# Kernel optimization log

Measured on AMD Instinct MI355X. Metric: run time of the kernel, lower is better.

The kernel has to match this reference:

```python
import jax, jax.numpy as jnp
import numpy as np

B, H, W, C = 2, 64, 64, 512
GROUPS = 32
EPS = 1e-5


def group_norm(x, gamma, beta):
    b, h, w, c = x.shape
    xg = x.reshape(b, h, w, GROUPS, c // GROUPS)
    mu = xg.mean(axis=(1, 2, 4), keepdims=True)
    var = xg.var(axis=(1, 2, 4), keepdims=True)
    xn = ((xg - mu) * jax.lax.rsqrt(var + EPS)).reshape(b, h, w, c)
    return xn * gamma + beta


def setup_inputs() -> dict:
    key = jax.random.key(0)
    ks = jax.random.split(key, 12)
    wscale = 0.02
    inputs = jax.random.normal(ks[0], (B, H, W, C), jnp.float32)
    gamma = jnp.ones((C,), jnp.float32)
    beta = jnp.zeros((C,), jnp.float32)
    Wq = jax.random.normal(ks[1], (C, C), jnp.float32) * wscale
    bq = jnp.zeros((C,), jnp.float32)
    Wk = jax.random.normal(ks[2], (C, C), jnp.float32) * wscale
    bk = jnp.zeros((C,), jnp.float32)
    Wv = jax.random.normal(ks[3], (C, C), jnp.float32) * wscale
    bv = jnp.zeros((C,), jnp.float32)
    Wp = jax.random.normal(ks[4], (C, C), jnp.float32) * wscale
    bp = jnp.zeros((C,), jnp.float32)
    return {"inputs": inputs, "gamma": gamma, "beta": beta,
            "Wq": Wq, "bq": bq, "Wk": Wk, "bk": bk,
            "Wv": Wv, "bv": bv, "Wp": Wp, "bp": bp}


def reference(inputs, gamma, beta, Wq, bq, Wk, bk, Wv, bv, Wp, bp):
    b, h, w, c = inputs.shape
    x = group_norm(inputs, gamma, beta)
    # QKV projections on [b, h, w, c], flatten spatial to sequence hw
    q = (x @ Wq + bq).reshape(b, h * w, c)
    k = (x @ Wk + bk).reshape(b, h * w, c)
    v = (x @ Wv + bv).reshape(b, h * w, c)
    scale = 1.0 / jnp.sqrt(jnp.asarray(c, q.dtype))
    # y[b,i,j] = <q_i, k_j> / sqrt(c); softmax over keys j (last axis, keras default)
    attn = jax.nn.softmax(jnp.einsum('bqc,bkc->bqk', q, k) * scale, axis=-1)
    # out_i = sum_j attn[i,j] * v_j  (matches v @ y^T in the original)
    o = jnp.einsum('bqk,bkc->bqc', attn, v).reshape(b, h, w, c)
    return (o @ Wp + bp) + inputs
```

## Files before the change

### kernel.cpp

```cpp
#include <hip/hip_runtime.h>
#include <hip/hip_bf16.h>
#include <cstddef>


typedef __bf16 bf16;
typedef __attribute__((ext_vector_type(8))) __bf16 bf16x8;
typedef __attribute__((ext_vector_type(4))) __bf16 bf16x4;
typedef __attribute__((ext_vector_type(4))) float f32x4;

#define SEQ   4096
#define CCH   512
#define NBAT  2
#define NOMASK 0x7FFFFFFF
#define SMEM_BYTES 32768

__device__ __forceinline__ void prep_unit(
    char* smem, int bid, const float* __restrict__ x,
    const float* __restrict__ Wq, const float* __restrict__ Wk,
    const float* __restrict__ Wv, const float* __restrict__ Wp,
    const float* __restrict__ bq, const float* __restrict__ bk,
    const float* __restrict__ bv,
    float* __restrict__ statsP, bf16* __restrict__ WqkvT,
    bf16* __restrict__ WpT, float* __restrict__ biasQKV) {
    const int tid = threadIdx.x;
    if (bid < 512) {
        float* red = (float*)smem;
        int bg = bid >> 3, c = bid & 7;
        int b = bg >> 5, g = bg & 31;
        const float* base = x + (size_t)b * SEQ * CCH + g * 16;
        float s = 0.f, ss = 0.f;
        for (int i = tid; i < 2048; i += 256) {
            int sp = c * 512 + (i >> 2), q = i & 3;
            float4 v = *(const float4*)(base + (size_t)sp * CCH + q * 4);
            s  += v.x + v.y + v.z + v.w;
            ss += v.x * v.x + v.y * v.y + v.z * v.z + v.w * v.w;
        }
        #pragma unroll
        for (int o = 32; o > 0; o >>= 1) { s += __shfl_down(s, o); ss += __shfl_down(ss, o); }
        int wave = tid >> 6, lane = tid & 63;
        if (lane == 0) { red[wave] = s; red[4 + wave] = ss; }
        __syncthreads();
        if (tid == 0) {
            statsP[bg * 16 + c]     = red[0] + red[1] + red[2] + red[3];
            statsP[bg * 16 + 8 + c] = red[4] + red[5] + red[6] + red[7];
        }
        __syncthreads();
    } else if (bid < 1536) {
        float (*tile)[33] = (float(*)[33])smem;
        int w = bid - 512;
        int z = w >> 8, rest = w & 255;
        int k0 = (rest >> 4) * 32, n0 = (rest & 15) * 32;
        const float* W = (z == 0) ? Wq : (z == 1) ? Wk : (z == 2) ? Wv : Wp;
        int tx = tid & 31, ty = tid >> 5;
        #pragma unroll
        for (int i = ty; i < 32; i += 8)
            tile[i][tx] = W[(size_t)(k0 + i) * CCH + n0 + tx];
        __syncthreads();
        bf16* dst = (z < 3) ? (WqkvT + (size_t)z * CCH * CCH) : WpT;
        #pragma unroll
        for (int i = ty; i < 32; i += 8)
            dst[(size_t)(n0 + i) * CCH + k0 + tx] = (bf16)tile[tx][i];
        __syncthreads();
    } else {
        for (int i = tid; i < 1536; i += 256) {
            float v = (i < 512) ? bq[i] : (i < 1024) ? bk[i - 512] : bv[i - 1024];
            biasQKV[i] = v;
        }
    }
}

__device__ __forceinline__ void gn_table(char* smem, const float* __restrict__ statsP) {
    float* tbl = (float*)smem;
    const int tid = threadIdx.x;
    if (tid < 64) {
        float S = 0.f, SS = 0.f;
        #pragma unroll
        for (int c = 0; c < 8; ++c) { S += statsP[tid * 16 + c]; SS += statsP[tid * 16 + 8 + c]; }
        float mu = S * (1.f / 65536.f);
        float rs = rsqrtf(SS * (1.f / 65536.f) - mu * mu + 1e-5f);
        tbl[tid * 2] = mu; tbl[tid * 2 + 1] = rs;
    }
    __syncthreads();
}

__device__ __forceinline__ void gn_unit(
    char* smem, int w, const float* __restrict__ x,
    const float* __restrict__ gamma, const float* __restrict__ beta,
    bf16* __restrict__ xn) {
    const float* tbl = (const float*)smem;
    size_t idx = (size_t)w * 256 + threadIdx.x;
    int c4 = (int)(idx & 127);
    int b = (int)(idx >> 19);
    int bg = b * 32 + (c4 >> 2);
    float mu = tbl[bg * 2], rs = tbl[bg * 2 + 1];
    float4 v  = ((const float4*)x)[idx];
    float4 gm = ((const float4*)gamma)[c4];
    float4 bt = ((const float4*)beta)[c4];
    bf16x4 o;
    o[0] = (bf16)((v.x - mu) * rs * gm.x + bt.x);
    o[1] = (bf16)((v.y - mu) * rs * gm.y + bt.y);
    o[2] = (bf16)((v.z - mu) * rs * gm.z + bt.z);
    o[3] = (bf16)((v.w - mu) * rs * gm.w + bt.w);
    ((bf16x4*)xn)[idx] = o;
}

__device__ __forceinline__ void vtrans_unit(char* smem,
                                            const bf16* __restrict__ qkv,
                                            bf16* __restrict__ vT,
                                            int b, int s0, int c0) {
    bf16 (*tile)[65] = (bf16(*)[65])smem;
    const int tx = threadIdx.x & 63;
    const int w = threadIdx.x >> 6;
    #pragma unroll
    for (int i = 0; i < 16; ++i) {
        int row = w + i * 4;
        tile[row][tx] = qkv[((size_t)b * SEQ + s0 + row) * 1536 + 1024 + c0 + tx];
    }
    __syncthreads();
    #pragma unroll
    for (int i = 0; i < 16; ++i) {
        int row = w + i * 4;
        vT[((size_t)b * CCH + c0 + row) * SEQ + s0 + tx] = tile[tx][row];
    }
    __syncthreads();
}

template <int EPI, int BN>
__device__ __forceinline__ void gemm2_body(
    char* smem, int bxi, int byi, int bzi,
    const bf16* __restrict__ A, long long aBatch, int lda,
    const bf16* __restrict__ Bt, long long bBatch, int ldb,
    void* __restrict__ Cout, long long cBatch, int ldc,
    int K, int bkmask, float scale,
    const float* __restrict__ bias, const float* __restrict__ resid,
    float* __restrict__ lsum, long long lsumBatch) {
    constexpr int JN = BN / 32;
    bf16* As = (bf16*)smem;
    bf16* Bs = (bf16*)(smem + 16384);
    const int tid = threadIdx.x;
    const int lane = tid & 63;
    const int wave = tid >> 6;

    int zb = bzi, kc = 0;
    if constexpr (EPI == 2) { kc = zb & 1; zb >>= 1; }
    const long long m0 = (long long)bxi * 128;
    const long long n0 = (long long)byi * BN;
    const bf16* Ab = A + (long long)zb * aBatch + (EPI == 2 ? (long long)kc * 2048 : 0);
    const bf16* Bb = Bt + (long long)zb * bBatch + (EPI == 2 ? (long long)kc * 2048 : 0);

    const int wm = (wave & 1) * 64;
    const int wn = (wave >> 1) * (BN / 2);
    const int fm = lane & 15;
    const int q4 = lane >> 4;

    f32x4 acc[4][JN];
    #pragma unroll
    for (int i = 0; i < 4; ++i)
        #pragma unroll
        for (int j = 0; j < JN; ++j)
            acc[i][j] = (f32x4){0.f, 0.f, 0.f, 0.f};

    const int srow = tid >> 3;
    const int schunk = (tid & 7) ^ (srow & 7);

    for (int k0 = 0; k0 < K; k0 += 64) {
        const int kA = k0 + schunk * 8;
        const int kB = (k0 & bkmask) + schunk * 8;
        #pragma unroll
        for (int cb = 0; cb < 4; ++cb) {
            const bf16* g = Ab + (m0 + cb * 32 + srow) * (long long)lda + kA;
            __builtin_amdgcn_global_load_lds((const __attribute__((address_space(1))) void*)g,
                                             (__attribute__((address_space(3))) void*)&As[cb * 2048 + tid * 8], 16, 0, 0);
        }
        #pragma unroll
        for (int cb = 0; cb < BN / 32; ++cb) {
            const bf16* g = Bb + (n0 + cb * 32 + srow) * (long long)ldb + kB;
            __builtin_amdgcn_global_load_lds((const __attribute__((address_space(1))) void*)g,
                                             (__attribute__((address_space(3))) void*)&Bs[cb * 2048 + tid * 8], 16, 0, 0);
        }
        __syncthreads();
        #pragma unroll
        for (int kcc = 0; kcc < 2; ++kcc) {
            bf16x8 fa[4], fb[JN];
            #pragma unroll
            for (int i = 0; i < 4; ++i) {
                const int row = wm + i * 16 + fm;
                const int sw = ((kcc * 4 + q4) ^ (fm & 7)) * 8;
                fa[i] = *(const bf16x8*)&As[row * 64 + sw];
            }
            #pragma unroll
            for (int j = 0; j < JN; ++j) {
                const int row = wn + j * 16 + fm;
                const int sw = ((kcc * 4 + q4) ^ (fm & 7)) * 8;
                fb[j] = *(const bf16x8*)&Bs[row * 64 + sw];
            }
            #pragma unroll
            for (int i = 0; i < 4; ++i)
                #pragma unroll
                for (int j = 0; j < JN; ++j)
                    acc[i][j] = __builtin_amdgcn_mfma_f32_16x16x32_bf16(fa[i], fb[j], acc[i][j], 0, 0, 0);
        }
        __syncthreads();
    }

    float* lrow = (float*)(smem + 1024);
    if constexpr (EPI == 2) {
        float* lscr = (float*)smem;
        const float* lsb = lsum + (long long)zb * lsumBatch + m0;
        const int row = tid & 127, h = tid >> 7;
        float s = 0.f;
        #pragma unroll
        for (int p = 0; p < 32; ++p)
            s += lsb[(long long)(h * 32 + p) * SEQ + row];
        lscr[tid] = s;
        __syncthreads();
        if (tid < 128) lrow[tid] = 1.f / (lscr[tid] + lscr[tid + 128]);
        __syncthreads();
    }

    const int col = lane & 15;
    const int rowb = (lane >> 4) * 4;

    if constexpr (EPI == 1) {
        bf16* Pb = (bf16*)Cout + (long long)zb * cBatch;
        float* lsw = lsum + (long long)zb * lsumBatch
                   + ((long long)byi * 2 + (wave >> 1)) * SEQ;
        #pragma unroll
        for (int i = 0; i < 4; ++i) {
            float rs[4] = {0.f, 0.f, 0.f, 0.f};
            long long mg = m0 + wm + i * 16 + rowb;
            #pragma unroll
            for (int j = 0; j < JN; ++j) {
                long long ng = n0 + wn + j * 16 + col;
                #pragma unroll
                for (int r = 0; r < 4; ++r) {
                    float e = __expf(acc[i][j][r] * scale);
                    rs[r] += e;
                    Pb[(mg + r) * (long long)ldc + ng] = (bf16)e;
                }
            }
            #pragma unroll
            for (int r = 0; r < 4; ++r) {
                rs[r] += __shfl_xor(rs[r], 1);
                rs[r] += __shfl_xor(rs[r], 2);
                rs[r] += __shfl_xor(rs[r], 4);
                rs[r] += __shfl_xor(rs[r], 8);
            }
            if (col == 0) {
                #pragma unroll
                for (int r = 0; r < 4; ++r) lsw[mg + r] = rs[r];
            }
        }
    } else {
        #pragma unroll
        for (int i = 0; i < 4; ++i) {
            #pragma unroll
            for (int j = 0; j < JN; ++j) {
                long long mg = m0 + wm + i * 16 + rowb;
                long long ng = n0 + wn + j * 16 + col;
                #pragma unroll
                for (int r = 0; r < 4; ++r) {
                    float v = acc[i][j][r];
                    long long m = mg + r;
                    if constexpr (EPI == 0) {
                        ((bf16*)Cout)[m * (long long)ldc + ng] = (bf16)(v + bias[ng]);
                    } else if constexpr (EPI == 2) {
                        float inv = lrow[(int)(m - m0)];
                        ((bf16*)Cout)[(long long)zb * cBatch + m * (long long)ldc
                                      + kc * 512 + ng] = (bf16)(v * inv);
                    } else {
                        ((float*)Cout)[m * (long long)ldc + ng] =
                            v + bias[ng] + resid[m * CCH + ng];
                    }
                }
            }
        }
    }
}

__global__ __launch_bounds__(512, 2) void k_qk256(
    const bf16* __restrict__ qkv, bf16* __restrict__ P,
    float* __restrict__ lsum, float scale) {
    __shared__ __align__(16) bf16 lds[2][2][256 * 64];

    const int tid  = threadIdx.x;
    const int lane = tid & 63;
    const int wave = tid >> 6;
    const int qm = (wave >> 2) & 1;
    const int qn = wave & 3;
    const int fm = lane & 15;
    const int q4 = lane >> 4;

    const int bid = blockIdx.x;
    const int xcd = bid & 7, l = bid >> 3;
    const int bz = xcd >> 2, quad = xcd & 3;
    const int mt = (quad >> 1) * 8 + (l >> 3);
    const int nt = (quad & 1) * 8 + (l & 7);
    const long long m0 = (long long)mt * 256;
    const long long n0 = (long long)nt * 256;
    const bf16* Aq = qkv + (long long)bz * SEQ * 1536;
    const bf16* Bk = Aq + 512;

    const int srow = tid >> 3;
    const int schunk = tid & 7;

    f32x4 acc[4][4][2];
    #pragma unroll
    for (int p = 0; p < 4; ++p)
        #pragma unroll
        for (int i = 0; i < 4; ++i)
            #pragma unroll
            for (int j = 0; j < 2; ++j)
                acc[p][i][j] = (f32x4){0.f, 0.f, 0.f, 0.f};

    auto STAGE = [&](int h) {
        const int th = h >> 2, j = h & 3;
        const int half = j >> 1;
        const int ab = j & 1;
        const bf16* src = ab ? Bk : Aq;
        const long long base0 = ab ? n0 : m0;
        const int kc = th * 64 + ((schunk ^ (srow & 7)) << 3);
        bf16* dst = &lds[th & 1][ab][(half * 128) * 64];
        #pragma unroll
        for (int c = 0; c < 2; ++c) {
            const bf16* g = src + (base0 + half * 128 + c * 64 + srow) * 1536 + kc;
            __builtin_amdgcn_global_load_lds(
                (const __attribute__((address_space(1))) void*)g,
                (__attribute__((address_space(3))) void*)&dst[c * 64 * 64 + tid * 8],
                16, 0, 0);
        }
    };

    #pragma unroll
    for (int h = 0; h < 6; ++h) STAGE(h);
    asm volatile("s_waitcnt vmcnt(4)" ::: "memory");
    __builtin_amdgcn_sched_barrier(0);
    __builtin_amdgcn_s_barrier();
    __builtin_amdgcn_sched_barrier(0);

    #pragma unroll
    for (int T = 0; T < 8; ++T) {
        #pragma unroll
        for (int p = 0; p < 4; ++p) {
            const int mh = p >> 1, nh = p & 1, bi = T & 1;
            bf16x8 fa[4][2], fb[2][2];
            #pragma unroll
            for (int i = 0; i < 4; ++i) {
                const int R = mh * 128 + qm * 64 + i * 16 + fm;
                #pragma unroll
                for (int s = 0; s < 2; ++s)
                    fa[i][s] = *(const bf16x8*)
                        &lds[bi][0][R * 64 + ((((s << 2) + q4) ^ (fm & 7)) << 3)];
            }
            #pragma unroll
            for (int j = 0; j < 2; ++j) {
                const int R = nh * 128 + qn * 32 + j * 16 + fm;
                #pragma unroll
                for (int s = 0; s < 2; ++s)
                    fb[j][s] = *(const bf16x8*)
                        &lds[bi][1][R * 64 + ((((s << 2) + q4) ^ (fm & 7)) << 3)];
            }
            const int h = T * 4 + p + 6;
            if (h < 32) STAGE(h);
            __builtin_amdgcn_sched_barrier(0);
            __builtin_amdgcn_s_barrier();
            asm volatile("s_waitcnt lgkmcnt(0)" ::: "memory");
            __builtin_amdgcn_sched_barrier(0);
            __builtin_amdgcn_s_setprio(1);
            #pragma unroll
            for (int i = 0; i < 4; ++i)
                #pragma unroll
                for (int j = 0; j < 2; ++j)
                    #pragma unroll
                    for (int s = 0; s < 2; ++s)
                        acc[p][i][j] = __builtin_amdgcn_mfma_f32_16x16x32_bf16(
                            fa[i][s], fb[j][s], acc[p][i][j], 0, 0, 0);
            __builtin_amdgcn_s_setprio(0);
            __builtin_amdgcn_sched_barrier(0);
            if (p == 3 && T < 6)
                asm volatile("s_waitcnt vmcnt(4)" ::: "memory");
            else if (p == 3 && T == 6)
                asm volatile("s_waitcnt vmcnt(0)" ::: "memory");
            __builtin_amdgcn_sched_barrier(0);
            __builtin_amdgcn_s_barrier();
            __builtin_amdgcn_sched_barrier(0);
        }
    }

    const int col16 = lane & 15;
    const int rowb = (lane >> 4) * 4;
    bf16* Pb = P + (long long)bz * SEQ * SEQ;
    float* lsw = lsum + (long long)bz * 64 * SEQ + (long long)(nt * 4 + qn) * SEQ;
    #pragma unroll
    for (int mh = 0; mh < 2; ++mh) {
        #pragma unroll
        for (int i = 0; i < 4; ++i) {
            float rs[4] = {0.f, 0.f, 0.f, 0.f};
            const long long mg = m0 + mh * 128 + qm * 64 + i * 16 + rowb;
            #pragma unroll
            for (int nh = 0; nh < 2; ++nh) {
                const int p = mh * 2 + nh;
                #pragma unroll
                for (int j = 0; j < 2; ++j) {
                    const long long ng = n0 + nh * 128 + qn * 32 + j * 16 + col16;
                    #pragma unroll
                    for (int r = 0; r < 4; ++r) {
                        float e = __expf(acc[p][i][j][r] * scale);
                        rs[r] += e;
                        Pb[(mg + r) * (long long)SEQ + ng] = (bf16)e;
                    }
                }
            }
            #pragma unroll
            for (int r = 0; r < 4; ++r) {
                rs[r] += __shfl_xor(rs[r], 1);
                rs[r] += __shfl_xor(rs[r], 2);
                rs[r] += __shfl_xor(rs[r], 4);
                rs[r] += __shfl_xor(rs[r], 8);
            }
            if (col16 == 0) {
                #pragma unroll
                for (int r = 0; r < 4; ++r) lsw[mg + r] = rs[r];
            }
        }
    }
}

__global__ __launch_bounds__(256) void k_prep(
    const float* x, const float* Wq, const float* Wk, const float* Wv,
    const float* Wp, const float* bq, const float* bk, const float* bv,
    float* statsP, bf16* WqkvT, bf16* WpT, float* biasQKV) {
    __shared__ __align__(16) char smem[4352];
    prep_unit(smem, blockIdx.x, x, Wq, Wk, Wv, Wp, bq, bk, bv,
              statsP, WqkvT, WpT, biasQKV);
}

__global__ __launch_bounds__(256) void k_gn(
    const float* x, const float* statsP, const float* gamma,
    const float* beta, bf16* xn) {
    __shared__ __align__(16) char smem[512];
    gn_table(smem, statsP);
    gn_unit(smem, blockIdx.x, x, gamma, beta, xn);
}

__global__ __launch_bounds__(256, 2) void k_qkv_m(
    const bf16* xn, const bf16* WqkvT, bf16* qkv, const float* biasQKV) {
    __shared__ __align__(16) char smem[SMEM_BYTES];
    int w = blockIdx.x, l = w >> 3;
    gemm2_body<0, 128>(smem, (w & 7) * 8 + l / 12, l % 12, 0,
                       xn, 0, CCH, WqkvT, 0, CCH, qkv, 0, 1536,
                       CCH, NOMASK, 1.f, biasQKV, nullptr, nullptr, 0);
}

__global__ __launch_bounds__(256, 2) void k_vtrans_m(const bf16* qkv, bf16* vT) {
    __shared__ __align__(16) char smem[8448];
    int w = blockIdx.x, b = w >> 9, r = w & 511;
    vtrans_unit(smem, qkv, vT, b, (r >> 3) * 64, (r & 7) * 64);
}

__global__ __launch_bounds__(256, 2) void k_pv_m(
    const bf16* P, const bf16* vT, bf16* o2, float* lsum) {
    __shared__ __align__(16) char smem[SMEM_BYTES];
    int w = blockIdx.x, l = w >> 3;
    int S = (w & 7) * 16 + (l >> 3);
    gemm2_body<2, 64>(smem, S & 31, l & 7, S >> 5,
                      P, (long long)SEQ * SEQ, SEQ,
                      vT, (long long)CCH * SEQ, SEQ,
                      o2, (long long)SEQ * 1024, 1024,
                      2048, NOMASK, 1.f, nullptr, nullptr,
                      lsum, 64LL * SEQ);
}

__global__ __launch_bounds__(256, 2) void k_proj_m(
    const bf16* o2, const bf16* WpT, float* out, const float* bp,
    const float* x) {
    __shared__ __align__(16) char smem[SMEM_BYTES];
    int w = blockIdx.x, l = w >> 3;
    gemm2_body<3, 64>(smem, (w & 7) * 8 + (l >> 3), l & 7, 0,
                      o2, 0, 1024, WpT, 0, CCH, out, 0, CCH,
                      1024, 511, 1.f, bp, x, nullptr, 0);
}

template <int EPI, int BN>
__global__ __launch_bounds__(256, 2) void k_gemm2(
    const bf16* A, long long aBatch, int lda,
    const bf16* Bt, long long bBatch, int ldb,
    void* Cout, long long cBatch, int ldc,
    int K, int bkmask, float scale,
    const float* bias, const float* resid,
    float* lsum, long long lsumBatch) {
    __shared__ __align__(16) char smem[SMEM_BYTES];
    gemm2_body<EPI, BN>(smem, blockIdx.x, blockIdx.y, blockIdx.z,
                        A, aBatch, lda, Bt, bBatch, ldb, Cout, cBatch, ldc,
                        K, bkmask, scale, bias, resid, lsum, lsumBatch);
}

__global__ __launch_bounds__(256, 2) void k_qk_vtrans(
    const bf16* qkv, bf16* vT, bf16* P, float* lsum, float scale,
    int vtBlocks, long long qkBatch, long long pBatch, long long lsumBatch) {
    __shared__ __align__(16) char smem[SMEM_BYTES];
    const int bid = blockIdx.x;
    if (bid < vtBlocks) {
        int b = bid >> 9, r = bid & 511;
        vtrans_unit(smem, qkv, vT, b, (r >> 3) * 64, (r & 7) * 64);
    } else {
        int q = bid - vtBlocks;
        int bz = q >> 10, r = q & 1023;
        gemm2_body<1, 128>(smem, r >> 5, r & 31, bz,
                           qkv, qkBatch, 1536, qkv + 512, qkBatch, 1536,
                           P, pBatch, SEQ, CCH, NOMASK, scale,
                           nullptr, nullptr, lsum, lsumBatch);
    }
}

extern "C" void kernel_launch(void* const* d_in, const int* in_sizes, int n_in,
                              void* d_out, int out_size, void* d_ws, size_t ws_size,
                              hipStream_t stream) {
    const float* x     = (const float*)d_in[0];
    const float* gamma = (const float*)d_in[1];
    const float* beta  = (const float*)d_in[2];
    const float* Wq    = (const float*)d_in[3];
    const float* bq    = (const float*)d_in[4];
    const float* Wk    = (const float*)d_in[5];
    const float* bk    = (const float*)d_in[6];
    const float* Wv    = (const float*)d_in[7];
    const float* bv    = (const float*)d_in[8];
    const float* Wp    = (const float*)d_in[9];
    const float* bp    = (const float*)d_in[10];
    float* out = (float*)d_out;

    constexpr size_t OFF_STATS = 0;
    constexpr size_t OFF_BIAS  = 4096;
    constexpr size_t OFF_WQKVT = 12288;
    constexpr size_t OFF_WPT   = 1585152;
    constexpr size_t OFF_XN    = 2109440;
    constexpr size_t OFF_LSUM  = OFF_XN;
    constexpr size_t OFF_QKV   = 10498048;
    constexpr size_t OFF_O2    = OFF_QKV;
    constexpr size_t OFF_VT    = 35663872;
    constexpr size_t OFF_P     = 44052480;
    constexpr size_t NEED_FULL = OFF_P + (size_t)NBAT * SEQ * SEQ * 2;

    char* ws = (char*)d_ws;
    float* statsP  = (float*)(ws + OFF_STATS);
    float* biasQKV = (float*)(ws + OFF_BIAS);
    bf16*  WqkvT   = (bf16*)(ws + OFF_WQKVT);
    bf16*  WpT     = (bf16*)(ws + OFF_WPT);
    bf16*  xn      = (bf16*)(ws + OFF_XN);
    float* lsum    = (float*)(ws + OFF_LSUM);
    bf16*  qkv     = (bf16*)(ws + OFF_QKV);
    bf16*  o2      = (bf16*)(ws + OFF_O2);
    bf16*  vT      = (bf16*)(ws + OFF_VT);
    bf16*  P       = (bf16*)(ws + OFF_P);

    const float scale = 0.044194173824159216f;
    const bool full = ws_size >= NEED_FULL;

    if (full) {
        k_prep<<<1537, 256, 0, stream>>>(x, Wq, Wk, Wv, Wp, bq, bk, bv,
                                         statsP, WqkvT, WpT, biasQKV);
        k_gn<<<4096, 256, 0, stream>>>(x, statsP, gamma, beta, xn);
        k_qkv_m<<<768, 256, 0, stream>>>(xn, WqkvT, qkv, biasQKV);
        k_vtrans_m<<<1024, 256, 0, stream>>>(qkv, vT);
        k_qk256<<<512, 512, 0, stream>>>(qkv, P, lsum, scale);
        k_pv_m<<<1024, 256, 0, stream>>>(P, vT, o2, lsum);
        k_proj_m<<<512, 256, 0, stream>>>(o2, WpT, out, bp, x);
    } else {
        k_prep<<<1537, 256, 0, stream>>>(x, Wq, Wk, Wv, Wp, bq, bk, bv,
                                         statsP, WqkvT, WpT, biasQKV);
        k_gn<<<4096, 256, 0, stream>>>(x, statsP, gamma, beta, xn);
        k_gemm2<0, 128><<<dim3(64, 12, 1), 256, 0, stream>>>(
            xn, 0, CCH, WqkvT, 0, CCH, qkv, 0, 1536,
            CCH, NOMASK, 1.f, biasQKV, nullptr, nullptr, 0);
        for (int b = 0; b < NBAT; ++b) {
            const bf16* qb = qkv + (long long)b * SEQ * 1536;
            k_qk_vtrans<<<1536, 256, 0, stream>>>(
                qb, vT + (long long)b * CCH * SEQ, P,
                lsum + (long long)b * 64 * SEQ, scale, 512, 0, 0, 0);
            k_gemm2<2, 128><<<dim3(32, 4, 2), 256, 0, stream>>>(
                P, 0, SEQ, vT + (long long)b * CCH * SEQ, 0, SEQ,
                o2 + (long long)b * SEQ * 1024, 0, 1024,
                2048, NOMASK, 1.f, nullptr, nullptr,
                lsum + (long long)b * 64 * SEQ, 0);
        }
        k_gemm2<3, 64><<<dim3(64, 8, 1), 256, 0, stream>>>(
            o2, 0, 1024, WpT, 0, CCH, out, 0, CCH,
            1024, 511, 1.f, bp, x, nullptr, 0);
    }
}
```

Baseline: 218.0 us.

## Reuse LDS fragments across quadrants in the QK^T tile with snake ordering

Reorders the four sub-tile MFMA phases of the QK^T tile in a snake order (00, 01, 11, 10) so A and B fragments loaded from LDS are reused across consecutive phases instead of being reloaded each phase. The staging order is changed to match, so the needed halves arrive in that sequence. Several sched_barriers and per-phase lgkmcnt waits are dropped and the barrier count per step is reduced, which lowers LDS read traffic and sync overhead. Removing the explicit waits and scheduling barriers leaves ordering to the compiler, which carries a risk of races or worse instruction interleaving.

```diff
diff --git a/kernel.cpp b/kernel.cpp
--- a/kernel.cpp
+++ b/kernel.cpp
@@ -314,9 +314,9 @@
                 acc[p][i][j] = (f32x4){0.f, 0.f, 0.f, 0.f};
 
     auto STAGE = [&](int h) {
-        const int th = h >> 2, j = h & 3;
-        const int half = j >> 1;
-        const int ab = j & 1;
+        const int th = h >> 2, jj = h & 3;
+        const int ab = (jj == 1 || jj == 2) ? 1 : 0;
+        const int half = jj & 1;
         const bf16* src = ab ? Bk : Aq;
         const long long base0 = ab ? n0 : m0;
         const int kc = th * 64 + ((schunk ^ (srow & 7)) << 3);
@@ -334,57 +334,100 @@
     #pragma unroll
     for (int h = 0; h < 6; ++h) STAGE(h);
     asm volatile("s_waitcnt vmcnt(4)" ::: "memory");
-    __builtin_amdgcn_sched_barrier(0);
     __builtin_amdgcn_s_barrier();
-    __builtin_amdgcn_sched_barrier(0);
 
     #pragma unroll
     for (int T = 0; T < 8; ++T) {
-        #pragma unroll
-        for (int p = 0; p < 4; ++p) {
-            const int mh = p >> 1, nh = p & 1, bi = T & 1;
-            bf16x8 fa[4][2], fb[2][2];
-            #pragma unroll
-            for (int i = 0; i < 4; ++i) {
-                const int R = mh * 128 + qm * 64 + i * 16 + fm;
+        const int bi = T & 1;
+        bf16x8 fa[4][2], fbA[2][2], fbB[2][2];
+
+        #pragma unroll
+        for (int i = 0; i < 4; ++i) {
+            const int R = qm * 64 + i * 16 + fm;
+            #pragma unroll
+            for (int s = 0; s < 2; ++s)
+                fa[i][s] = *(const bf16x8*)
+                    &lds[bi][0][R * 64 + ((((s << 2) + q4) ^ (fm & 7)) << 3)];
+        }
+        #pragma unroll
+        for (int j = 0; j < 2; ++j) {
+            const int R = qn * 32 + j * 16 + fm;
+            #pragma unroll
+            for (int s = 0; s < 2; ++s)
+                fbA[j][s] = *(const bf16x8*)
+                    &lds[bi][1][R * 64 + ((((s << 2) + q4) ^ (fm & 7)) << 3)];
+        }
+        if (T < 7) STAGE(T * 4 + 6);
+        __builtin_amdgcn_s_setprio(1);
+        #pragma unroll
+        for (int i = 0; i < 4; ++i)
+            #pragma unroll
+            for (int j = 0; j < 2; ++j)
                 #pragma unroll
                 for (int s = 0; s < 2; ++s)
-                    fa[i][s] = *(const bf16x8*)
-                        &lds[bi][0][R * 64 + ((((s << 2) + q4) ^ (fm & 7)) << 3)];
-            }
-            #pragma unroll
-            for (int j = 0; j < 2; ++j) {
-                const int R = nh * 128 + qn * 32 + j * 16 + fm;
+                    acc[0][i][j] = __builtin_amdgcn_mfma_f32_16x16x32_bf16(
+                        fa[i][s], fbA[j][s], acc[0][i][j], 0, 0, 0);
+        __builtin_amdgcn_s_setprio(0);
+        __builtin_amdgcn_s_barrier();
+
+        #pragma unroll
+        for (int j = 0; j < 2; ++j) {
+            const int R = 128 + qn * 32 + j * 16 + fm;
+            #pragma unroll
+            for (int s = 0; s < 2; ++s)
+                fbB[j][s] = *(const bf16x8*)
+                    &lds[bi][1][R * 64 + ((((s << 2) + q4) ^ (fm & 7)) << 3)];
+        }
+        if (T < 7) STAGE(T * 4 + 7);
+        __builtin_amdgcn_s_setprio(1);
+        #pragma unroll
+        for (int i = 0; i < 4; ++i)
+            #pragma unroll
+            for (int j = 0; j < 2; ++j)
                 #pragma unroll
                 for (int s = 0; s < 2; ++s)
-                    fb[j][s] = *(const bf16x8*)
-                        &lds[bi][1][R * 64 + ((((s << 2) + q4) ^ (fm & 7)) << 3)];
-            }
-            const int h = T * 4 + p + 6;
-            if (h < 32) STAGE(h);
-            __builtin_amdgcn_sched_barrier(0);
-            __builtin_amdgcn_s_barrier();
-            asm volatile("s_waitcnt lgkmcnt(0)" ::: "memory");
-            __builtin_amdgcn_sched_barrier(0);
-            __builtin_amdgcn_s_setprio(1);
-            #pragma unroll
-            for (int i = 0; i < 4; ++i)
-                #pragma unroll
-                for (int j = 0; j < 2; ++j)
-                    #pragma unroll
-                    for (int s = 0; s < 2; ++s)
-                        acc[p][i][j] = __builtin_amdgcn_mfma_f32_16x16x32_bf16(
-                            fa[i][s], fb[j][s], acc[p][i][j], 0, 0, 0);
-            __builtin_amdgcn_s_setprio(0);
-            __builtin_amdgcn_sched_barrier(0);
-            if (p == 3 && T < 6)
-                asm volatile("s_waitcnt vmcnt(4)" ::: "memory");
-            else if (p == 3 && T == 6)
-                asm volatile("s_waitcnt vmcnt(0)" ::: "memory");
-            __builtin_amdgcn_sched_barrier(0);
-            __builtin_amdgcn_s_barrier();
-            __builtin_amdgcn_sched_barrier(0);
-        }
+                    acc[1][i][j] = __builtin_amdgcn_mfma_f32_16x16x32_bf16(
+                        fa[i][s], fbB[j][s], acc[1][i][j], 0, 0, 0);
+        __builtin_amdgcn_s_setprio(0);
+        __builtin_amdgcn_s_barrier();
+
+        #pragma unroll
+        for (int i = 0; i < 4; ++i) {
+            const int R = 128 + qm * 64 + i * 16 + fm;
+            #pragma unroll
+            for (int s = 0; s < 2; ++s)
+                fa[i][s] = *(const bf16x8*)
+                    &lds[bi][0][R * 64 + ((((s << 2) + q4) ^ (fm & 7)) << 3)];
+        }
+        if (T < 6) STAGE(T * 4 + 8);
+        __builtin_amdgcn_s_setprio(1);
+        #pragma unroll
+        for (int i = 0; i < 4; ++i)
+            #pragma unroll
+            for (int j = 0; j < 2; ++j)
+                #pragma unroll
+                for (int s = 0; s < 2; ++s)
+                    acc[3][i][j] = __builtin_amdgcn_mfma_f32_16x16x32_bf16(
+                        fa[i][s], fbB[j][s], acc[3][i][j], 0, 0, 0);
+        __builtin_amdgcn_s_setprio(0);
+        __builtin_amdgcn_s_barrier();
+
+        if (T < 6) STAGE(T * 4 + 9);
+        __builtin_amdgcn_s_setprio(1);
+        #pragma unroll
+        for (int i = 0; i < 4; ++i)
+            #pragma unroll
+            for (int j = 0; j < 2; ++j)
+                #pragma unroll
+                for (int s = 0; s < 2; ++s)
+                    acc[2][i][j] = __builtin_amdgcn_mfma_f32_16x16x32_bf16(
+                        fa[i][s], fbA[j][s], acc[2][i][j], 0, 0, 0);
+        __builtin_amdgcn_s_setprio(0);
+        if (T < 6)
+            asm volatile("s_waitcnt vmcnt(4)" ::: "memory");
+        else if (T == 6)
+            asm volatile("s_waitcnt vmcnt(0)" ::: "memory");
+        if (T < 7) __builtin_amdgcn_s_barrier();
     }
 
     const int col16 = lane & 15;
```

Measured after the change: 221.8 us. About the same (+1.7%).
